# Kernel tuning notes

Hardware: AMD Instinct MI355X
Metric: run time of the kernel (lower is better)

## Reference

```python
import jax, jax.numpy as jnp
import numpy as np
import math

# neuralef_loss_cfg constants
T = 10.0
K_FEAT = 32          # num_nearestn_feature
K_PIX = ((10, 2.0), (10, 0.1))  # (num_nearestn_pixel{1,2}, distance_weight)
PIX_W = 0.05         # pixelwise_weight
ALPHA = 1.0


def setup_inputs() -> dict:
    key = jax.random.key(0)
    k1, k2, k3 = jax.random.split(key, 3)
    highlevel_feature = jax.random.normal(k1, (8, 1024, 768), dtype=jnp.float32)
    Psi = jax.random.normal(k2, (8, 1024, 64), dtype=jnp.float32)
    im = jax.random.normal(k3, (8, 3, 32, 32), dtype=jnp.float32)
    return {"highlevel_feature": highlevel_feature, "Psi": Psi, "im": im}


def _build_gram(highlevel_feature, im):
    """Feature kNN graph + pixel kNN graphs -> degree-normalized gram matrix."""
    bs, n, d = highlevel_feature.shape
    M = bs * n
    # --- feature affinity: cosine sim, mutual-ish kNN sparsification ---
    X = highlevel_feature.reshape(M, d)
    X = X / jnp.linalg.norm(X, axis=-1, keepdims=True)
    A = X @ X.T                                   # [M, M]
    A = A.at[jnp.diag_indices(M)].set(-jnp.inf)
    A = jnp.maximum(A, 0.0)                       # clamp(min=0); diag -inf -> 0
    vals, idx = jax.lax.top_k(A, K_FEAT)          # [M, K]
    res = jnp.zeros_like(A).at[jnp.arange(M)[:, None], idx].set(vals)
    A = (res + res.T) * 0.5

    # --- pixel affinity: RGB + weighted xy coordinates, euclidean kNN ---
    im = (im + 1.0) / 2.0
    h, w = im.shape[2], im.shape[3]
    hw = h * w
    x_ = jnp.tile(jnp.linspace(0.0, 1.0, w), (h,))          # [hw]
    y_ = jnp.repeat(jnp.linspace(0.0, 1.0, h), w)           # [hw]
    imf = im.reshape(bs, 3, hw).transpose(0, 2, 1)          # [bs, hw, 3]
    row = jnp.arange(hw)
    A_p = jnp.zeros((bs, hw, hw), dtype=bool)
    for k, dw in K_PIX:
        if k == 0:
            continue
        coords = jnp.broadcast_to(jnp.stack([x_ * dw, y_ * dw], -1), (bs, hw, 2))
        im2 = jnp.concatenate([imf, coords], axis=-1)       # [bs, hw, 5]
        sq = jnp.sum(im2 * im2, axis=-1)                    # [bs, hw]
        d2 = sq[:, :, None] + sq[:, None, :] - 2.0 * jnp.einsum('bnd,bmd->bnm', im2, im2)
        euc = -jnp.sqrt(jnp.maximum(d2, 0.0))               # -cdist
        euc = euc.at[:, row, row].set(-jnp.inf)
        _, pidx = jax.lax.top_k(euc, k)                     # [bs, hw, k]
        r = jnp.zeros((bs, hw, hw), dtype=bool).at[
            jnp.arange(bs)[:, None, None], row[None, :, None], pidx].set(True)
        A_p = A_p | r | r.transpose(0, 2, 1)

    A2 = jax.scipy.linalg.block_diag(*[A_p[i].astype(jnp.float32) for i in range(bs)])

    D = jax.lax.rsqrt(A.sum(-1))
    gram = A * D[None, :] * D[:, None]
    D2 = jax.lax.rsqrt(A2.sum(-1))
    gram2 = A2 * D2[None, :] * D2[:, None]
    return gram + gram2 * PIX_W                             # [M, M]


def reference(highlevel_feature, Psi, im):
    Psi = Psi.reshape(-1, Psi.shape[-1]) * math.sqrt(T)     # [M, kdim]
    gram = _build_gram(highlevel_feature, im)
    gP = gram @ Psi                                         # [M, kdim]
    R = Psi.T @ gP
    R_hat = jax.lax.stop_gradient(Psi).T @ gP               # no_sg = False
    kdim = Psi.shape[1]
    loss = -jnp.trace(R) / kdim
    reg = jnp.sum(jnp.triu(R_hat ** 2, 1)) / kdim
    return (loss, reg * ALPHA)
```

## Files before the change

### kernel.cpp

```cpp
#include <hip/hip_runtime.h>
#include <hip/hip_bf16.h>
#include <math.h>

constexpr int MT  = 8192;
constexpr int DF  = 768;
constexpr int KD  = 64;
constexpr int HWP = 1024;
constexpr int KF  = 32;
constexpr int KP  = 10;
constexpr int RPB = 256;
constexpr int CAP   = 24;
constexpr int CANDQ = 512;
#define SQT 3.16227766016837933f
#define PIXW 0.05f
#define THR_BITS 0x2C7Bu

typedef __bf16 bf16x8 __attribute__((ext_vector_type(8)));
typedef __bf16 bf16x4 __attribute__((ext_vector_type(4)));
typedef float  f32x4  __attribute__((ext_vector_type(4)));
typedef unsigned u32x4 __attribute__((ext_vector_type(4)));
typedef unsigned short u16x8 __attribute__((ext_vector_type(8)));
typedef _Float16 f16;

__global__ __launch_bounds__(256) void prep_input_kernel(const float* __restrict__ X,
                                                         __bf16* __restrict__ Xb,
                                                         const float* __restrict__ im,
                                                         unsigned* __restrict__ pmask) {
  __shared__ float fr[HWP], fg[HWP], fb[HWP];
  __shared__ float red[256];
  const int tid = threadIdx.x;
  if (blockIdx.x < MT) {
    const int row = blockIdx.x;
    const float4* xr4 = (const float4*)(X + (size_t)row * DF);
    float4 v = make_float4(0.f, 0.f, 0.f, 0.f);
    float s = 0.f;
    if (tid < 192) {
      v = xr4[tid];
      s = v.x * v.x + v.y * v.y + v.z * v.z + v.w * v.w;
    }
    red[tid] = s; __syncthreads();
    for (int o = 128; o > 0; o >>= 1) { if (tid < o) red[tid] += red[tid + o]; __syncthreads(); }
    const float rn = rsqrtf(red[0]);
    if (tid < 192) {
      bf16x4 o;
      o[0] = (__bf16)(v.x * rn); o[1] = (__bf16)(v.y * rn);
      o[2] = (__bf16)(v.z * rn); o[3] = (__bf16)(v.w * rn);
      *(bf16x4*)(Xb + (size_t)row * DF + tid * 4) = o;
    }
    return;
  }
  const int bx = blockIdx.x - MT;
  const int lane = tid & 63, wv = tid >> 6;
  const int b = bx >> 8;
  const int p = ((bx & 255) << 2) + wv;
  const float* imb = im + (size_t)b * 3 * HWP;
  for (int q = tid; q < HWP; q += 256) {
    fr[q] = imb[q]; fg[q] = imb[HWP + q]; fb[q] = imb[2 * HWP + q];
  }
  __syncthreads();
  const float pr = fr[p], pg = fg[p], pb = fb[p];
  const float px = (float)(p & 31) * (1.f / 31.f), py = (float)(p >> 5) * (1.f / 31.f);
  float d0[16], d1[16];
  #pragma unroll
  for (int i = 0; i < 16; ++i) {
    const int q = lane + (i << 6);
    float dr = (fr[q] - pr) * 0.5f, dg = (fg[q] - pg) * 0.5f, db = (fb[q] - pb) * 0.5f;
    float drgb = dr * dr + dg * dg + db * db;
    float dx = (float)(q & 31) * (1.f / 31.f) - px;
    float dy = (float)(q >> 5) * (1.f / 31.f) - py;
    float cd = dx * dx + dy * dy;
    d0[i] = (q == p) ? 1e30f : drgb + 4.00f * cd;
    d1[i] = (q == p) ? 1e30f : drgb + 0.01f * cd;
  }
  const int mrow = (b << 10) + p;
  auto doPass = [&](float (&dd)[16]) {
    for (int it = 0; it < KP; ++it) {
      float bm = 1e30f; int bq = 0;
      #pragma unroll
      for (int i = 0; i < 16; ++i) {
        const int q = lane + (i << 6);
        if (dd[i] < bm) { bm = dd[i]; bq = q; }
      }
      #pragma unroll
      for (int o = 32; o > 0; o >>= 1) {
        float ov = __shfl_down(bm, o);
        int   oq = __shfl_down(bq, o);
        if (ov < bm) { bm = ov; bq = oq; }
      }
      bq = __shfl(bq, 0);
      if (lane == 0) {
        atomicOr(&pmask[(size_t)mrow * 32 + (bq >> 5)], 1u << (bq & 31));
        atomicOr(&pmask[((size_t)((b << 10) + bq)) * 32 + (p >> 5)], 1u << (p & 31));
      }
      #pragma unroll
      for (int i = 0; i < 16; ++i)
        if (lane + (i << 6) == bq) dd[i] = 1e30f;
    }
  };
  doPass(d0);
  doPass(d1);
}

union SMem {
  struct { __bf16 A[128 * 64]; __bf16 B[128 * 64]; } st;
  f16 T[128 * 128];
};

__global__ __launch_bounds__(256) void gemm_kernel(const __bf16* __restrict__ Xb,
                                                   unsigned* __restrict__ cnt2,
                                                   unsigned* __restrict__ cand) {
  __shared__ SMem sm;
  const int tid = threadIdx.x;
  const int lane = tid & 63;
  const int wv = tid >> 6;
  const int wm = (wv & 1) * 64, wn = (wv >> 1) * 64;
  const int l15 = lane & 15, lq = lane >> 4;
  const int lr8 = lane >> 3, lc8 = lane & 7;
  const int rsw = l15 & 7;

  const int xcd = blockIdx.x & 7;
  const int s = blockIdx.x >> 3;
  const int p = s / 65, r = s % 65;
  const int c1 = xcd * 4 + p;
  int ti, tj;
  if (r <= c1) { ti = r; tj = c1; }
  else         { ti = r - c1 - 1; tj = 63 - c1; }
  const int m0 = ti * 128;
  const int n0 = tj * 128;

  f32x4 acc[4][4];
  #pragma unroll
  for (int i = 0; i < 4; ++i)
    #pragma unroll
    for (int j = 0; j < 4; ++j)
      #pragma unroll
      for (int q = 0; q < 4; ++q) acc[i][j][q] = 0.f;

  for (int kt = 0; kt < 12; ++kt) {
    const int col0 = kt * 64;
    const __bf16* Ag = Xb + (size_t)m0 * DF + col0;
    const __bf16* Bg = Xb + (size_t)n0 * DF + col0;
    #pragma unroll
    for (int i = 0; i < 4; ++i) {
      const int r0 = (wv * 4 + i) * 8;
      const int csw = (lc8 ^ lr8) * 8;
      __builtin_amdgcn_global_load_lds(
          (const __attribute__((address_space(1))) void*)(Ag + (size_t)(r0 + lr8) * DF + csw),
          (__attribute__((address_space(3))) void*)(&sm.st.A[r0 * 64]), 16, 0, 0);
      __builtin_amdgcn_global_load_lds(
          (const __attribute__((address_space(1))) void*)(Bg + (size_t)(r0 + lr8) * DF + csw),
          (__attribute__((address_space(3))) void*)(&sm.st.B[r0 * 64]), 16, 0, 0);
    }
    __syncthreads();
    #pragma unroll
    for (int kk = 0; kk < 64; kk += 32) {
      bf16x8 af[4], bg[4];
      #pragma unroll
      for (int i = 0; i < 4; ++i)
        af[i] = *(const bf16x8*)(&sm.st.A[(wm + i * 16 + l15) * 64 + ((((kk >> 3) + lq) ^ rsw) * 8)]);
      #pragma unroll
      for (int j = 0; j < 4; ++j)
        bg[j] = *(const bf16x8*)(&sm.st.B[(wn + j * 16 + l15) * 64 + ((((kk >> 3) + lq) ^ rsw) * 8)]);
      #pragma unroll
      for (int i = 0; i < 4; ++i)
        #pragma unroll
        for (int j = 0; j < 4; ++j)
          acc[i][j] = __builtin_amdgcn_mfma_f32_16x16x32_bf16(af[i], bg[j], acc[i][j], 0, 0, 0);
    }
    __syncthreads();
  }

  const bool offdiag = (m0 != n0);
  const int lane16 = tid & 15;

  auto scan_phase = [&](int outBase, int partnerBase, int tIdx, bool isdiag) {
    for (int e = tid; e < 128 * 16; e += 256) {
      const int rr = e >> 4, ch = e & 15;
      const u16x8 vv = *(const u16x8*)&sm.T[rr * 128 + ((ch ^ (rr & 7)) << 3)];
      unsigned msk = 0;
      #pragma unroll
      for (int k = 0; k < 8; ++k) {
        const unsigned u = vv[k];
        if (u >= THR_BITS && u < 0x8000u) msk |= 1u << k;
      }
      if (isdiag) {
        const int kx = rr - ch * 8;
        if (kx >= 0 && kx < 8) msk &= ~(1u << kx);
      }
      const int cnt = __popc(msk);
      int x = cnt;
      #pragma unroll
      for (int o = 1; o < 16; o <<= 1) {
        const int y = __shfl_up(x, o);
        if (lane16 >= o) x += y;
      }
      const int gr = outBase + rr;
      int pos = x - cnt;
      const size_t slab = ((size_t)gr * 64 + tIdx) * (size_t)CAP;
      unsigned m2 = msk;
      while (m2) {
        const int k = __ffs(m2) - 1; m2 &= m2 - 1;
        if (pos < CAP) {
          const unsigned pk = ((unsigned)vv[k] << 16) | (unsigned)(8191 - (partnerBase + ch * 8 + k));
          __builtin_nontemporal_store(pk, &cand[slab + pos]);
        }
        ++pos;
      }
      if (lane16 == 15)
        __builtin_nontemporal_store((unsigned)min(x, CAP), &cnt2[(size_t)gr * 64 + tIdx]);
    }
  };

  #pragma unroll
  for (int i = 0; i < 4; ++i)
    #pragma unroll
    for (int j = 0; j < 4; ++j)
      #pragma unroll
      for (int q = 0; q < 4; ++q) {
        const int tr = wm + i * 16 + lq * 4 + q;
        const int tc = wn + j * 16 + l15;
        sm.T[tr * 128 + ((((tc >> 3) ^ (tr & 7)) << 3) | (tc & 7))] = (f16)acc[i][j][q];
      }
  __syncthreads();
  scan_phase(m0, n0, tj, !offdiag);

  if (offdiag) {
    __syncthreads();
    #pragma unroll
    for (int i = 0; i < 4; ++i)
      #pragma unroll
      for (int j = 0; j < 4; ++j)
        #pragma unroll
        for (int q = 0; q < 4; ++q) {
          const int tr = wm + i * 16 + lq * 4 + q;
          const int tc = wn + j * 16 + l15;
          sm.T[tc * 128 + ((((tr >> 3) ^ (tc & 7)) << 3) | (tr & 7))] = (f16)acc[i][j][q];
        }
    __syncthreads();
    scan_phase(n0, m0, ti, false);
  }
}

__global__ __launch_bounds__(256) void select_kernel(const unsigned* __restrict__ cnt2,
                                                     const unsigned* __restrict__ cand,
                                                     int* __restrict__ fidx,
                                                     float* __restrict__ fval,
                                                     float* __restrict__ frow) {
  __shared__ unsigned cp[CANDQ];
  __shared__ int off[65];
  const int tid = threadIdx.x;
  const int row = blockIdx.x;
  if (tid == 0) { frow[row] = 0.f; off[0] = 0; }
  if (tid < 64) {
    int x = (int)cnt2[(size_t)row * 64 + tid];
    #pragma unroll
    for (int o = 1; o < 64; o <<= 1) {
      const int y = __shfl_up(x, o);
      if (tid >= o) x += y;
    }
    off[tid + 1] = x;
  }
  __syncthreads();
  const int n = min(off[64], CANDQ);
  {
    const int t = tid >> 2, k0 = tid & 3;
    const int o0 = off[t], ct = off[t + 1] - o0;
    const unsigned* slab = &cand[((size_t)row * 64 + t) * CAP];
    for (int k = k0; k < ct; k += 4)
      if (o0 + k < CANDQ) cp[o0 + k] = slab[k];
  }
  __syncthreads();
  for (int e = tid; e < n; e += 256) {
    const unsigned me = cp[e];
    int rank = 0;
    for (int j = 0; j < n; ++j) rank += (cp[j] > me);
    if (rank < KF) {
      union { unsigned short u; f16 h; } cv; cv.u = (unsigned short)(me >> 16);
      fval[(size_t)row * KF + rank] = (float)cv.h;
      fidx[(size_t)row * KF + rank] = 8191 - (int)(me & 0x1fffu);
    }
  }
  for (int rk = n + tid; rk < KF; rk += 256) {
    fval[(size_t)row * KF + rk] = 0.f;
    fidx[(size_t)row * KF + rk] = row;
  }
}

typedef unsigned u32x4v __attribute__((ext_vector_type(4)));
__global__ void feat_deg_kernel(const int* __restrict__ fidx, const float* __restrict__ fval,
                                float* __restrict__ frow) {
  int m = blockIdx.x * blockDim.x + threadIdx.x;
  if (m >= MT) return;
  float s = 0.f;
  for (int k = 0; k < KF; ++k) {
    float v = fval[m * KF + k];
    s += v;
    atomicAdd(&frow[fidx[m * KF + k]], 0.5f * v);
  }
  atomicAdd(&frow[m], 0.5f * s);
}

__global__ void scales_kernel(const float* __restrict__ frow,
                              const unsigned* __restrict__ pmask,
                              float* __restrict__ sf, float* __restrict__ sp,
                              float* __restrict__ Rm) {
  int m = blockIdx.x * blockDim.x + threadIdx.x;
  if (m < KD * KD) Rm[m] = 0.f;
  if (m >= MT) return;
  const u32x4* pm = (const u32x4*)(pmask + (size_t)m * 32);
  int deg = 0;
  #pragma unroll
  for (int w = 0; w < 8; ++w) {
    const u32x4 bits = pm[w];
    deg += __popc(bits[0]) + __popc(bits[1]) + __popc(bits[2]) + __popc(bits[3]);
  }
  const float fr = frow[m];
  sf[m] = (fr > 0.f) ? rsqrtf(fr) * SQT : 0.f;
  sp[m] = (deg > 0) ? rsqrtf((float)deg) * SQT : 0.f;
}

__global__ __launch_bounds__(64) void gather_kernel(const int* __restrict__ fidx,
                                                    const float* __restrict__ fval,
                                                    const float* __restrict__ sf,
                                                    const float* __restrict__ sp,
                                                    const unsigned* __restrict__ pmask,
                                                    const float* __restrict__ Psi,
                                                    float* __restrict__ Wf,
                                                    float* __restrict__ W2) {
  __shared__ int list[64];
  __shared__ int cnt;
  const int m = blockIdx.x;
  const int t = threadIdx.x;
  const int b = m >> 10;
  if (t == 0) cnt = 0;
  __syncthreads();
  if (t < 32) {
    unsigned bits = pmask[(size_t)m * 32 + t];
    while (bits) {
      int bit = __ffs(bits) - 1;
      bits &= bits - 1;
      int pos = atomicAdd(&cnt, 1);
      if (pos < 64) list[pos] = t * 32 + bit;
    }
  }
  __syncthreads();
  float accf = 0.f;
  for (int k = 0; k < KF; ++k) {
    const float v = fval[m * KF + k];
    const int   c = fidx[m * KF + k];
    accf += 0.5f * v * sf[c] * Psi[(size_t)c * KD + t];
  }
  Wf[(size_t)m * KD + t] = accf;
  const int n = min(cnt, 64);
  float accp = 0.f;
  for (int e = 0; e < n; ++e) {
    const int g = b * HWP + list[e];
    accp += sp[g] * Psi[(size_t)g * KD + t];
  }
  W2[(size_t)m * KD + t] = accp;
}

__global__ __launch_bounds__(256) void rmat_part_kernel(const float* __restrict__ Psi,
                                                        const float* __restrict__ sf,
                                                        const float* __restrict__ sp,
                                                        const float* __restrict__ Wf,
                                                        const float* __restrict__ W2,
                                                        float* __restrict__ Pf,
                                                        float* __restrict__ Pp) {
  __shared__ float sPsi[8][KD], sWf[8][KD], sW2[8][KD];
  __shared__ float ssf[8], ssp[8];
  const int tid = threadIdx.x;
  const int c = tid & 63, g = tid >> 6;
  float accf[16], accp[16];
  #pragma unroll
  for (int i = 0; i < 16; ++i) { accf[i] = 0.f; accp[i] = 0.f; }
  const int rowBeg = blockIdx.x * (MT / RPB);
  for (int r0 = rowBeg; r0 < rowBeg + MT / RPB; r0 += 8) {
    #pragma unroll
    for (int e = tid; e < 8 * KD; e += 256) {
      const int r = e >> 6, cc = e & 63;
      const size_t gi = (size_t)(r0 + r) * KD + cc;
      sPsi[r][cc] = Psi[gi];
      sWf[r][cc]  = Wf[gi];
      sW2[r][cc]  = W2[gi];
    }
    if (tid < 8) { ssf[tid] = sf[r0 + tid]; ssp[tid] = sp[r0 + tid]; }
    __syncthreads();
    #pragma unroll
    for (int r = 0; r < 8; ++r) {
      const float wf = sWf[r][c], w2 = sW2[r][c];
      const float fsc = ssf[r], psc = ssp[r];
      const f32x4* p4 = (const f32x4*)&sPsi[r][g * 16];
      #pragma unroll
      for (int q = 0; q < 4; ++q) {
        const f32x4 pp = p4[q];
        #pragma unroll
        for (int k = 0; k < 4; ++k) {
          accf[q * 4 + k] += fsc * pp[k] * wf;
          accp[q * 4 + k] += psc * pp[k] * w2;
        }
      }
    }
    __syncthreads();
  }
  float* pf = Pf + (size_t)blockIdx.x * KD * KD;
  float* pp = Pp + (size_t)blockIdx.x * KD * KD;
  #pragma unroll
  for (int i = 0; i < 16; ++i) {
    const int a = g * 16 + i;
    pf[a * KD + c] = accf[i];
    pp[a * KD + c] = accp[i];
  }
}

__global__ __launch_bounds__(256) void rmat_reduce_kernel(const float* __restrict__ Pf,
                                                          const float* __restrict__ Pp,
                                                          float* __restrict__ Rm) {
  const int e = (blockIdx.x & 15) * 256 + threadIdx.x;
  const int grp = blockIdx.x >> 4;
  const int a = e >> 6, c = e & 63;
  const int eT = c * KD + a;
  float f = 0.f, ft = 0.f, p = 0.f;
  #pragma unroll 8
  for (int b = grp * 64; b < grp * 64 + 64; ++b) {
    f  += Pf[(size_t)b * KD * KD + e];
    ft += Pf[(size_t)b * KD * KD + eT];
    p  += Pp[(size_t)b * KD * KD + e];
  }
  atomicAdd(&Rm[e], f + ft + PIXW * p);
}

__global__ __launch_bounds__(256) void final_kernel(const float* __restrict__ Rm,
                                                    float* __restrict__ out) {
  __shared__ float redt[256], redr[256];
  const int tid = threadIdx.x;
  float tr = 0.f, rg = 0.f;
  for (int e = tid; e < KD * KD; e += 256) {
    int a = e >> 6, c = e & 63;
    float v = Rm[e];
    if (a == c) tr += v;
    else if (c > a) rg += v * v;
  }
  redt[tid] = tr; redr[tid] = rg;
  __syncthreads();
  for (int o = 128; o > 0; o >>= 1) {
    if (tid < o) { redt[tid] += redt[tid + o]; redr[tid] += redr[tid + o]; }
    __syncthreads();
  }
  if (tid == 0) {
    out[0] = -redt[0] / (float)KD;
    out[1] = redr[0] / (float)KD;
  }
}

extern "C" void kernel_launch(void* const* d_in, const int* in_sizes, int n_in,
                              void* d_out, int out_size, void* d_ws, size_t ws_size,
                              hipStream_t stream) {
  const float* hl  = (const float*)d_in[0];
  const float* Psi = (const float*)d_in[1];
  const float* im  = (const float*)d_in[2];
  float* out = (float*)d_out;

  char* ws = (char*)d_ws;
  size_t off = 0;
  auto alloc = [&](size_t bytes) -> void* {
    void* p = ws + off;
    off = (off + bytes + 255) & ~(size_t)255;
    return p;
  };
  unsigned* cand  = (unsigned*)alloc((size_t)MT * 64 * CAP * 4);
  unsigned* cnt2  = (unsigned*)alloc((size_t)MT * 64 * 4);
  __bf16*   Xb    = (__bf16*)alloc((size_t)MT * DF * 2);
  int*      fidx  = (int*)alloc((size_t)MT * KF * 4);
  float*    fval  = (float*)alloc((size_t)MT * KF * 4);
  float*    frow  = (float*)alloc((size_t)MT * 4);
  float*    sf    = (float*)alloc((size_t)MT * 4);
  float*    sp    = (float*)alloc((size_t)MT * 4);
  unsigned* pmask = (unsigned*)alloc((size_t)MT * 32 * 4);
  float*    Wf    = (float*)alloc((size_t)MT * KD * 4);
  float*    W2    = (float*)alloc((size_t)MT * KD * 4);
  float*    Pf    = (float*)alloc((size_t)RPB * KD * KD * 4);
  float*    Pp    = (float*)alloc((size_t)RPB * KD * KD * 4);
  float*    Rm    = (float*)alloc((size_t)KD * KD * 4);

  hipMemsetAsync(pmask, 0, (size_t)MT * 32 * 4, stream);

  prep_input_kernel<<<MT + MT / 4, 256, 0, stream>>>(hl, Xb, im, pmask);
  gemm_kernel<<<2080, 256, 0, stream>>>(Xb, cnt2, cand);
  select_kernel<<<MT, 256, 0, stream>>>(cnt2, cand, fidx, fval, frow);
  feat_deg_kernel<<<MT / 256, 256, 0, stream>>>(fidx, fval, frow);
  scales_kernel<<<MT / 256, 256, 0, stream>>>(frow, pmask, sf, sp, Rm);
  gather_kernel<<<MT, 64, 0, stream>>>(fidx, fval, sf, sp, pmask, Psi, Wf, W2);
  rmat_part_kernel<<<RPB, 256, 0, stream>>>(Psi, sf, sp, Wf, W2, Pf, Pp);
  rmat_reduce_kernel<<<64, 256, 0, stream>>>(Pf, Pp, Rm);
  final_kernel<<<1, 256, 0, stream>>>(Rm, out);
}
```

Before: 339.5 us.

## Split GEMM candidate scan into separate compact kernel, fuse degree accumulation into select

The GEMM kernel now writes each 128x128 fp16 similarity tile to a global scratch buffer instead of scanning it in place. A new compact kernel reloads each tile, extracts above-threshold candidates for both the row and the transposed direction, and writes them out. The aim is to relieve the GEMM kernel of the scan's register and LDS pressure and its divergent stores. Separately, the feature-degree accumulation moves into select_kernel with atomics, dropping feat_deg_kernel, and gather_kernel packs four rows per 256-thread block. The cost is an extra round trip of about 68MB of fp16 tiles through global memory, plus one more launch.

Result: no change. 340.8 us (+0.4%).

```diff
diff --git a/kernel.cpp b/kernel.cpp
--- a/kernel.cpp
+++ b/kernel.cpp
@@ -11,6 +11,7 @@
 constexpr int RPB = 256;
 constexpr int CAP   = 24;
 constexpr int CANDQ = 512;
+constexpr int NTILE = 2080;
 #define SQT 3.16227766016837933f
 #define PIXW 0.05f
 #define THR_BITS 0x2C7Bu
@@ -22,15 +23,29 @@
 typedef unsigned short u16x8 __attribute__((ext_vector_type(8)));
 typedef _Float16 f16;
 
+__device__ inline void tile_map(int bid, int& ti, int& tj) {
+  const int xcd = bid & 7;
+  const int s = bid >> 3;
+  const int p = s / 65, r = s % 65;
+  const int c1 = xcd * 4 + p;
+  if (r <= c1) { ti = r; tj = c1; }
+  else         { ti = r - c1 - 1; tj = 63 - c1; }
+}
+__device__ inline int tile_idx(int ti, int tj) {
+  return ti * 64 - (ti * (ti - 1)) / 2 + (tj - ti);
+}
+
 __global__ __launch_bounds__(256) void prep_input_kernel(const float* __restrict__ X,
                                                          __bf16* __restrict__ Xb,
                                                          const float* __restrict__ im,
-                                                         unsigned* __restrict__ pmask) {
+                                                         unsigned* __restrict__ pmask,
+                                                         float* __restrict__ frow) {
   __shared__ float fr[HWP], fg[HWP], fb[HWP];
   __shared__ float red[256];
   const int tid = threadIdx.x;
   if (blockIdx.x < MT) {
     const int row = blockIdx.x;
+    if (tid == 0) frow[row] = 0.f;
     const float4* xr4 = (const float4*)(X + (size_t)row * DF);
     float4 v = make_float4(0.f, 0.f, 0.f, 0.f);
     float s = 0.f;
@@ -107,8 +122,7 @@
 };
 
 __global__ __launch_bounds__(256) void gemm_kernel(const __bf16* __restrict__ Xb,
-                                                   unsigned* __restrict__ cnt2,
-                                                   unsigned* __restrict__ cand) {
+                                                   f16* __restrict__ Sp) {
   __shared__ SMem sm;
   const int tid = threadIdx.x;
   const int lane = tid & 63;
@@ -118,13 +132,8 @@
   const int lr8 = lane >> 3, lc8 = lane & 7;
   const int rsw = l15 & 7;
 
-  const int xcd = blockIdx.x & 7;
-  const int s = blockIdx.x >> 3;
-  const int p = s / 65, r = s % 65;
-  const int c1 = xcd * 4 + p;
   int ti, tj;
-  if (r <= c1) { ti = r; tj = c1; }
-  else         { ti = r - c1 - 1; tj = 63 - c1; }
+  tile_map(blockIdx.x, ti, tj);
   const int m0 = ti * 128;
   const int n0 = tj * 128;
 
@@ -169,48 +178,6 @@
     }
     __syncthreads();
   }
-
-  const bool offdiag = (m0 != n0);
-  const int lane16 = tid & 15;
-
-  auto scan_phase = [&](int outBase, int partnerBase, int tIdx, bool isdiag) {
-    for (int e = tid; e < 128 * 16; e += 256) {
-      const int rr = e >> 4, ch = e & 15;
-      const u16x8 vv = *(const u16x8*)&sm.T[rr * 128 + ((ch ^ (rr & 7)) << 3)];
-      unsigned msk = 0;
-      #pragma unroll
-      for (int k = 0; k < 8; ++k) {
-        const unsigned u = vv[k];
-        if (u >= THR_BITS && u < 0x8000u) msk |= 1u << k;
-      }
-      if (isdiag) {
-        const int kx = rr - ch * 8;
-        if (kx >= 0 && kx < 8) msk &= ~(1u << kx);
-      }
-      const int cnt = __popc(msk);
-      int x = cnt;
-      #pragma unroll
-      for (int o = 1; o < 16; o <<= 1) {
-        const int y = __shfl_up(x, o);
-        if (lane16 >= o) x += y;
-      }
-      const int gr = outBase + rr;
-      int pos = x - cnt;
-      const size_t slab = ((size_t)gr * 64 + tIdx) * (size_t)CAP;
-      unsigned m2 = msk;
-      while (m2) {
-        const int k = __ffs(m2) - 1; m2 &= m2 - 1;
-        if (pos < CAP) {
-          const unsigned pk = ((unsigned)vv[k] << 16) | (unsigned)(8191 - (partnerBase + ch * 8 + k));
-          __builtin_nontemporal_store(pk, &cand[slab + pos]);
-        }
-        ++pos;
-      }
-      if (lane16 == 15)
-        __builtin_nontemporal_store((unsigned)min(x, CAP), &cnt2[(size_t)gr * 64 + tIdx]);
-    }
-  };
-
   #pragma unroll
   for (int i = 0; i < 4; ++i)
     #pragma unroll
@@ -222,22 +189,99 @@
         sm.T[tr * 128 + ((((tc >> 3) ^ (tr & 7)) << 3) | (tc & 7))] = (f16)acc[i][j][q];
       }
   __syncthreads();
-  scan_phase(m0, n0, tj, !offdiag);
-
-  if (offdiag) {
+  {
+    f16* tile = Sp + (size_t)tile_idx(ti, tj) * (128 * 128);
+    for (int e = tid; e < 128 * 16; e += 256) {
+      const int r = e >> 4, ch = e & 15;
+      const u32x4 v = *(const u32x4*)&sm.T[r * 128 + ((ch ^ (r & 7)) << 3)];
+      __builtin_nontemporal_store(v, (u32x4*)&tile[r * 128 + ch * 8]);
+    }
+  }
+}
+
+constexpr int TS = 136;
+__global__ __launch_bounds__(256) void compact_kernel(const f16* __restrict__ Sp,
+                                                      unsigned* __restrict__ cnt2,
+                                                      unsigned* __restrict__ cand) {
+  __shared__ f16 T[128 * TS];
+  const int tid = threadIdx.x;
+  const int lane16 = tid & 15;
+  int ti, tj;
+  tile_map(blockIdx.x, ti, tj);
+  const int m0 = ti * 128, n0 = tj * 128;
+  const bool isdiag = (ti == tj);
+  const f16* tile = Sp + (size_t)tile_idx(ti, tj) * (128 * 128);
+
+  for (int e = tid; e < 128 * 16; e += 256) {
+    const int rr = e >> 4, ch = e & 15;
+    const u32x4 v = *(const u32x4*)&tile[(size_t)e * 8];
+    *(u32x4*)&T[rr * TS + ch * 8] = v;
+    const u16x8 vv = __builtin_bit_cast(u16x8, v);
+    unsigned msk = 0;
+    #pragma unroll
+    for (int k = 0; k < 8; ++k) {
+      const unsigned u = vv[k];
+      if (u >= THR_BITS && u < 0x8000u) msk |= 1u << k;
+    }
+    if (isdiag) {
+      const int kx = rr - ch * 8;
+      if (kx >= 0 && kx < 8) msk &= ~(1u << kx);
+    }
+    const int cnt = __popc(msk);
+    int x = cnt;
+    #pragma unroll
+    for (int o = 1; o < 16; o <<= 1) {
+      const int y = __shfl_up(x, o);
+      if (lane16 >= o) x += y;
+    }
+    const int gr = m0 + rr;
+    int pos = x - cnt;
+    const size_t slab = ((size_t)gr * 64 + tj) * CAP;
+    unsigned m2 = msk;
+    while (m2) {
+      const int k = __ffs(m2) - 1; m2 &= m2 - 1;
+      if (pos < CAP)
+        __builtin_nontemporal_store(((unsigned)vv[k] << 16) | (unsigned)(8191 - (n0 + ch * 8 + k)),
+                                    &cand[slab + pos]);
+      ++pos;
+    }
+    if (lane16 == 15)
+      __builtin_nontemporal_store((unsigned)min(x, CAP), &cnt2[(size_t)gr * 64 + tj]);
+  }
+  if (!isdiag) {
     __syncthreads();
-    #pragma unroll
-    for (int i = 0; i < 4; ++i)
-      #pragma unroll
-      for (int j = 0; j < 4; ++j)
-        #pragma unroll
-        for (int q = 0; q < 4; ++q) {
-          const int tr = wm + i * 16 + lq * 4 + q;
-          const int tc = wn + j * 16 + l15;
-          sm.T[tc * 128 + ((((tr >> 3) ^ (tc & 7)) << 3) | (tr & 7))] = (f16)acc[i][j][q];
-        }
-    __syncthreads();
-    scan_phase(n0, m0, ti, false);
+    for (int e = tid; e < 128 * 16; e += 256) {
+      const int rr = e >> 4, ch = e & 15;
+      unsigned short us[8];
+      unsigned msk = 0;
+      #pragma unroll
+      for (int k = 0; k < 8; ++k) {
+        const int kk = (k + lane16) & 7;
+        const unsigned u = __builtin_bit_cast(unsigned short, T[(ch * 8 + kk) * TS + rr]);
+        us[kk] = (unsigned short)u;
+        if (u >= THR_BITS && u < 0x8000u) msk |= 1u << kk;
+      }
+      const int cnt = __popc(msk);
+      int x = cnt;
+      #pragma unroll
+      for (int o = 1; o < 16; o <<= 1) {
+        const int y = __shfl_up(x, o);
+        if (lane16 >= o) x += y;
+      }
+      const int gr = n0 + rr;
+      int pos = x - cnt;
+      const size_t slab = ((size_t)gr * 64 + ti) * CAP;
+      unsigned m2 = msk;
+      while (m2) {
+        const int k = __ffs(m2) - 1; m2 &= m2 - 1;
+        if (pos < CAP)
+          __builtin_nontemporal_store(((unsigned)us[k] << 16) | (unsigned)(8191 - (m0 + ch * 8 + k)),
+                                      &cand[slab + pos]);
+        ++pos;
+      }
+      if (lane16 == 15)
+        __builtin_nontemporal_store((unsigned)min(x, CAP), &cnt2[(size_t)gr * 64 + ti]);
+    }
   }
 }
 
@@ -248,9 +292,10 @@
                                                      float* __restrict__ frow) {
   __shared__ unsigned cp[CANDQ];
   __shared__ int off[65];
+  __shared__ float srow;
   const int tid = threadIdx.x;
   const int row = blockIdx.x;
-  if (tid == 0) { frow[row] = 0.f; off[0] = 0; }
+  if (tid == 0) { off[0] = 0; srow = 0.f; }
   if (tid < 64) {
     int x = (int)cnt2[(size_t)row * 64 + tid];
     #pragma unroll
@@ -275,29 +320,21 @@
     int rank = 0;
     for (int j = 0; j < n; ++j) rank += (cp[j] > me);
     if (rank < KF) {
-      union { unsigned short u; f16 h; } cv; cv.u = (unsigned short)(me >> 16);
-      fval[(size_t)row * KF + rank] = (float)cv.h;
-      fidx[(size_t)row * KF + rank] = 8191 - (int)(me & 0x1fffu);
+      union { unsigned short u; f16 h; } cvu; cvu.u = (unsigned short)(me >> 16);
+      const float vv = (float)cvu.h;
+      const int idx = 8191 - (int)(me & 0x1fffu);
+      fval[(size_t)row * KF + rank] = vv;
+      fidx[(size_t)row * KF + rank] = idx;
+      atomicAdd(&frow[idx], 0.5f * vv);
+      atomicAdd(&srow, 0.5f * vv);
     }
   }
   for (int rk = n + tid; rk < KF; rk += 256) {
     fval[(size_t)row * KF + rk] = 0.f;
     fidx[(size_t)row * KF + rk] = row;
   }
-}
-
-typedef unsigned u32x4v __attribute__((ext_vector_type(4)));
-__global__ void feat_deg_kernel(const int* __restrict__ fidx, const float* __restrict__ fval,
-                                float* __restrict__ frow) {
-  int m = blockIdx.x * blockDim.x + threadIdx.x;
-  if (m >= MT) return;
-  float s = 0.f;
-  for (int k = 0; k < KF; ++k) {
-    float v = fval[m * KF + k];
-    s += v;
-    atomicAdd(&frow[fidx[m * KF + k]], 0.5f * v);
-  }
-  atomicAdd(&frow[m], 0.5f * s);
+  __syncthreads();
+  if (tid == 0) atomicAdd(&frow[row], srow);
 }
 
 __global__ void scales_kernel(const float* __restrict__ frow,
@@ -319,28 +356,29 @@
   sp[m] = (deg > 0) ? rsqrtf((float)deg) * SQT : 0.f;
 }
 
-__global__ __launch_bounds__(64) void gather_kernel(const int* __restrict__ fidx,
-                                                    const float* __restrict__ fval,
-                                                    const float* __restrict__ sf,
-                                                    const float* __restrict__ sp,
-                                                    const unsigned* __restrict__ pmask,
-                                                    const float* __restrict__ Psi,
-                                                    float* __restrict__ Wf,
-                                                    float* __restrict__ W2) {
-  __shared__ int list[64];
-  __shared__ int cnt;
-  const int m = blockIdx.x;
-  const int t = threadIdx.x;
+__global__ __launch_bounds__(256) void gather_kernel(const int* __restrict__ fidx,
+                                                     const float* __restrict__ fval,
+                                                     const float* __restrict__ sf,
+                                                     const float* __restrict__ sp,
+                                                     const unsigned* __restrict__ pmask,
+                                                     const float* __restrict__ Psi,
+                                                     float* __restrict__ Wf,
+                                                     float* __restrict__ W2) {
+  __shared__ int list[4][64];
+  __shared__ int cnts[4];
+  const int w = threadIdx.x >> 6;
+  const int t = threadIdx.x & 63;
+  const int m = blockIdx.x * 4 + w;
   const int b = m >> 10;
-  if (t == 0) cnt = 0;
+  if (t == 0) cnts[w] = 0;
   __syncthreads();
   if (t < 32) {
     unsigned bits = pmask[(size_t)m * 32 + t];
     while (bits) {
       int bit = __ffs(bits) - 1;
       bits &= bits - 1;
-      int pos = atomicAdd(&cnt, 1);
-      if (pos < 64) list[pos] = t * 32 + bit;
+      int pos = atomicAdd(&cnts[w], 1);
+      if (pos < 64) list[w][pos] = t * 32 + bit;
     }
   }
   __syncthreads();
@@ -351,10 +389,10 @@
     accf += 0.5f * v * sf[c] * Psi[(size_t)c * KD + t];
   }
   Wf[(size_t)m * KD + t] = accf;
-  const int n = min(cnt, 64);
+  const int n = min(cnts[w], 64);
   float accp = 0.f;
   for (int e = 0; e < n; ++e) {
-    const int g = b * HWP + list[e];
+    const int g = b * HWP + list[w][e];
     accp += sp[g] * Psi[(size_t)g * KD + t];
   }
   W2[(size_t)m * KD + t] = accp;
@@ -468,6 +506,7 @@
     off = (off + bytes + 255) & ~(size_t)255;
     return p;
   };
+  f16*      Sp    = (f16*)alloc((size_t)NTILE * 128 * 128 * 2);
   unsigned* cand  = (unsigned*)alloc((size_t)MT * 64 * CAP * 4);
   unsigned* cnt2  = (unsigned*)alloc((size_t)MT * 64 * 4);
   __bf16*   Xb    = (__bf16*)alloc((size_t)MT * DF * 2);
@@ -485,12 +524,12 @@
 
   hipMemsetAsync(pmask, 0, (size_t)MT * 32 * 4, stream);
 
-  prep_input_kernel<<<MT + MT / 4, 256, 0, stream>>>(hl, Xb, im, pmask);
-  gemm_kernel<<<2080, 256, 0, stream>>>(Xb, cnt2, cand);
+  prep_input_kernel<<<MT + MT / 4, 256, 0, stream>>>(hl, Xb, im, pmask, frow);
+  gemm_kernel<<<NTILE, 256, 0, stream>>>(Xb, Sp);
+  compact_kernel<<<NTILE, 256, 0, stream>>>(Sp, cnt2, cand);
   select_kernel<<<MT, 256, 0, stream>>>(cnt2, cand, fidx, fval, frow);
-  feat_deg_kernel<<<MT / 256, 256, 0, stream>>>(fidx, fval, frow);
   scales_kernel<<<MT / 256, 256, 0, stream>>>(frow, pmask, sf, sp, Rm);
-  gather_kernel<<<MT, 64, 0, stream>>>(fidx, fval, sf, sp, pmask, Psi, Wf, W2);
+  gather_kernel<<<MT / 4, 256, 0, stream>>>(fidx, fval, sf, sp, pmask, Psi, Wf, W2);
   rmat_part_kernel<<<RPB, 256, 0, stream>>>(Psi, sf, sp, Wf, W2, Pf, Pp);
   rmat_reduce_kernel<<<64, 256, 0, stream>>>(Pf, Pp, Rm);
   final_kernel<<<1, 256, 0, stream>>>(Rm, out);
```
